# Optimization experiments

Measured on AMD Instinct MI355X. Metric: run time of the kernel, lower is better.

Reference implementation:

```python
import jax, jax.numpy as jnp
import numpy as np

B, CI, CO, K, SD, H, W = 8, 128, 128, 3, 512, 256, 256


def setup_inputs() -> dict:
    key = jax.random.key(0)
    k0, k1, k2, k3 = jax.random.split(key, 4)
    x = jax.random.normal(k0, (B, CI, H, W), jnp.float32)
    style = jax.random.normal(k1, (B, SD), jnp.float32)
    # learned params
    w_base = jax.random.normal(k2, (1, CO, CI, K, K), jnp.float32)   # ModulatedConv2d.weight
    aff_w = jax.random.normal(k3, (CI, SD), jnp.float32)             # affine weight [out=CI, in=SD]
    aff_b = jnp.ones((CI,), jnp.float32)                             # bias_init=1
    return {"x": x, "style": style, "w_base": w_base, "aff_w": aff_w, "aff_b": aff_b}


def reference(x, style, w_base, aff_w, aff_b):
    b, ci, h, w_ = x.shape
    co, k = w_base.shape[1], w_base.shape[3]
    # affine: FullyConnectedLayer, linear activation, weight_gain = 1/sqrt(style_dim)
    aff_gain = 1.0 / np.sqrt(aff_w.shape[1])
    s = style @ (aff_w * aff_gain).T + aff_b                 # [B, CI]
    # modulate
    wgain = 1.0 / np.sqrt(ci * k * k)
    wt = w_base * wgain * s[:, None, :, None, None]          # [B, CO, CI, K, K]
    # demodulate
    d = jax.lax.rsqrt(jnp.sum(wt * wt, axis=(2, 3, 4)) + 1e-8)  # [B, CO]
    wt = wt * d[:, :, None, None, None]
    # grouped conv, groups = batch, padding = k//2 (up=down=1 path)
    wt = wt.reshape(b * co, ci, k, k)
    xg = x.reshape(1, b * ci, h, w_)
    pad = k // 2
    y = jax.lax.conv_general_dilated(
        xg, wt, window_strides=(1, 1), padding=[(pad, pad), (pad, pad)],
        dimension_numbers=("NCHW", "OIHW", "NCHW"), feature_group_count=b)
    return y.reshape(b, co, h, w_)
```

## Files before the change

kernel.cpp:

```cpp
#include <hip/hip_runtime.h>
#include <stdint.h>

#define BB 8
#define SD 512
#define PP 66564

typedef unsigned short u16;
typedef __attribute__((ext_vector_type(8))) __bf16 bf16x8;
typedef __attribute__((ext_vector_type(16))) float f32x16;

__device__ float g_s[BB * 128];
__device__ u16 g_wtb[BB * 9 * 2 * 8192];
__device__ u16 g_xb[(size_t)BB * 258 * 258 * 128 + 2048];

typedef const __attribute__((address_space(1))) uint32_t* gp1;
typedef __attribute__((address_space(3))) uint32_t* lp3;

__device__ __forceinline__ void glds16(const void* g, void* l) {
    __builtin_amdgcn_global_load_lds((gp1)g, (lp3)l, 16, 0, 0);
}
__device__ __forceinline__ void glds4(const void* g, void* l) {
    __builtin_amdgcn_global_load_lds((gp1)g, (lp3)l, 4, 0, 0);
}

__device__ __forceinline__ u16 f2bf(float f) {
    uint32_t u = __float_as_uint(f);
    u += 0x7FFFu + ((u >> 16) & 1u);
    return (u16)(u >> 16);
}

__global__ void affine_kernel(const float* __restrict__ style,
                              const float* __restrict__ aff_w,
                              const float* __restrict__ aff_b) {
    int b = blockIdx.x;
    int ci = threadIdx.x;
    const float gain = 0.044194173824159216f;
    const float* st = style + b * SD;
    const float* aw = aff_w + ci * SD;
    float acc = 0.f;
    #pragma unroll 8
    for (int j = 0; j < SD; ++j) acc += st[j] * aw[j];
    g_s[b * 128 + ci] = acc * gain + aff_b[ci];
}

__global__ __launch_bounds__(256) void modulate_kernel(const float* __restrict__ w_base) {
    int blk = blockIdx.x;
    int b = blk >> 7, co = blk & 127;
    int tid = threadIdx.x;
    const float wgain = 0.029462782549439483f;
    const int n = 1152;
    const float* wb = w_base + co * n;
    const float* sp = g_s + b * 128;

    float v[5];
    float sq = 0.f;
    #pragma unroll
    for (int i = 0; i < 5; ++i) {
        int idx = tid + i * 256;
        float w = 0.f;
        if (idx < n) {
            int ci = idx / 9;
            w = wb[idx] * wgain * sp[ci];
        }
        v[i] = w;
        sq += w * w;
    }
    #pragma unroll
    for (int off = 32; off > 0; off >>= 1) sq += __shfl_down(sq, off, 64);
    __shared__ float red[4];
    int lane = tid & 63, wvi = tid >> 6;
    if (lane == 0) red[wvi] = sq;
    __syncthreads();
    float tot = red[0] + red[1] + red[2] + red[3];
    float d = rsqrtf(tot + 1e-8f);
    #pragma unroll
    for (int i = 0; i < 5; ++i) {
        int idx = tid + i * 256;
        if (idx < n) {
            int ci = idx / 9;
            int k9 = idx - ci * 9;
            u16 hv = f2bf(v[i] * d);
            int slot = (ci & 63) >> 3, e = ci & 7;
            size_t base = ((size_t)(b * 9 + k9) * 2 + (ci >> 6)) * 8192;
            g_wtb[base + slot * 1024 + co * 8 + e] = hv;
        }
    }
}

__global__ __launch_bounds__(256) void zero_border_kernel() {
    int b = blockIdx.x;
    uint4 z = make_uint4(0, 0, 0, 0);
    char* xbB = (char*)g_xb;
    for (int i = threadIdx.x; i < 16448; i += 256) {
        int plane = i / 1028, rem = i - plane * 1028;
        int gy, gx;
        if (rem < 258)      { gy = 0;             gx = rem; }
        else if (rem < 516) { gy = 257;           gx = rem - 258; }
        else if (rem < 772) { gy = rem - 516 + 1; gx = 0; }
        else                { gy = rem - 772 + 1; gx = 257; }
        size_t a16 = (size_t)(b * 16 + plane) * PP + (size_t)gy * 258 + gx;
        *(uint4*)(xbB + a16 * 16) = z;
    }
}

__global__ __launch_bounds__(256) void transpose_kernel(const float* __restrict__ x) {
    __shared__ __align__(16) u16 t_lds[64 * 128];
    const int chunk = blockIdx.x;
    const int gy = blockIdx.y;
    const int b = blockIdx.z;
    const int px0 = chunk * 64;
    const int tid = threadIdx.x;
    const int pq = tid & 15;
    const int cig = tid >> 4;

    const float* base = x + (size_t)b * 128 * 65536 + (size_t)gy * 256 + px0 + pq * 4;
    char* ldsB = (char*)t_lds;

    float4 v[8];
    #pragma unroll
    for (int c = 0; c < 8; ++c)
        v[c] = *(const float4*)(base + (size_t)(cig * 8 + c) * 65536);

    #pragma unroll
    for (int j = 0; j < 4; ++j) {
        uint32_t dw[4];
        #pragma unroll
        for (int d = 0; d < 4; ++d) {
            const float* lo4 = (const float*)&v[2 * d];
            const float* hi4 = (const float*)&v[2 * d + 1];
            dw[d] = (uint32_t)f2bf(lo4[j]) | ((uint32_t)f2bf(hi4[j]) << 16);
        }
        int px = pq * 4 + j;
        int key = (px0 + px + 1) & 7;
        int slot = cig ^ key;
        *(uint4*)(ldsB + px * 256 + slot * 16) = *(uint4*)dw;
    }
    __syncthreads();

    char* outB = (char*)g_xb;
    #pragma unroll
    for (int it = 0; it < 4; ++it) {
        int flat = it * 256 + tid;
        int r = flat >> 4, k = flat & 15;
        int key = (px0 + r + 1) & 7;
        uint4 val = *(const uint4*)(ldsB + r * 256 + ((k ^ key) << 4));
        size_t a16 = (size_t)(b * 16 + k) * PP + (size_t)(gy + 1) * 258 + (px0 + r + 1);
        *(uint4*)(outB + a16 * 16) = val;
    }
}

__global__ __launch_bounds__(512, 4) void conv_kernel(float* __restrict__ y) {
    __shared__ __align__(16) u16 xs[2720 * 8];
    __shared__ __align__(16) u16 ab[2][8192];

    const int b = blockIdx.y;
    const int t = blockIdx.x;
    const int swzt = (t & 7) * 32 + (t >> 3);
    const int tx = swzt & 7, ty = swzt >> 3;
    const int y0 = ty * 8, x0 = tx * 32;
    const int tid = threadIdx.x;
    const int lane = tid & 63, wv = tid >> 6;
    const int l31 = lane & 31;
    const int l5 = lane >> 5;
    const int coHalf = (wv & 1) * 64;
    const int py0w = (wv >> 1) * 2;

    const char* xbB = (const char*)g_xb;
    const char* wtbB = (const char*)(g_wtb) + (size_t)b * 294912;
    char* xsB = (char*)xs;

    f32x16 acc[2][2];
    #pragma unroll
    for (int mf = 0; mf < 2; ++mf)
        #pragma unroll
        for (int rf = 0; rf < 2; ++rf)
            acc[mf][rf] = (f32x16){0.f};

    for (int h = 0; h < 2; ++h) {
        for (int i = wv; i < 44; i += 8) {
            if (i < 42) {
                int entry = i * 64 + lane;
                int slot = entry / 340;
                int rem = entry - slot * 340;
                int row = rem / 34;
                int col = rem - row * 34;
                size_t a16 = (size_t)(b * 16 + h * 8 + slot) * PP +
                             (size_t)(y0 + row) * 258 + (x0 + col);
                glds16(xbB + a16 * 16, xsB + i * 1024);
            } else {
                int j = i - 42;
                int entry = 2688 + j * 16 + (lane >> 2);
                int rem = entry - 2380;
                int row = rem / 34;
                int col = rem - row * 34;
                size_t a16 = (size_t)(b * 16 + h * 8 + 7) * PP +
                             (size_t)(y0 + row) * 258 + (x0 + col);
                glds4(xbB + a16 * 16 + (lane & 3) * 4, xsB + 43008 + j * 256);
            }
        }
        if (h == 0) {
            #pragma unroll
            for (int q = 0; q < 2; ++q) {
                int j = wv * 2 + q;
                glds16(wtbB + j * 1024 + lane * 16, (char*)ab[0] + j * 1024);
            }
        }
        __syncthreads();

        for (int tap = 0; tap < 9; ++tap) {
            int s = h * 9 + tap;
            if (s < 17) {
                int ns = s + 1;
                int ntap = (ns >= 9) ? (ns - 9) : ns;
                int nh = (ns >= 9) ? 1 : h;
                const char* src = wtbB + (ntap * 2 + nh) * 16384;
                char* dst = (char*)ab[ns & 1];
                #pragma unroll
                for (int q = 0; q < 2; ++q) {
                    int j = wv * 2 + q;
                    glds16(src + j * 1024 + lane * 16, dst + j * 1024);
                }
            }

            const int ky = tap / 3, kx = tap - ky * 3;
            const char* abuf = (const char*)ab[s & 1];
            const int brow = (py0w + ky) * 34 + l31 + kx;

            #pragma unroll
            for (int ks = 0; ks < 4; ++ks) {
                const int cig = ks * 2 + l5;
                bf16x8 af[2];
                #pragma unroll
                for (int mf = 0; mf < 2; ++mf) {
                    int co = coHalf + mf * 32 + l31;
                    af[mf] = *(const bf16x8*)(abuf + cig * 2048 + co * 16);
                }
                bf16x8 bf[2];
                #pragma unroll
                for (int rf = 0; rf < 2; ++rf)
                    bf[rf] = *(const bf16x8*)(xsB + (cig * 340 + brow + rf * 34) * 16);
                __builtin_amdgcn_s_setprio(1);
                #pragma unroll
                for (int mf = 0; mf < 2; ++mf)
                    #pragma unroll
                    for (int rf = 0; rf < 2; ++rf)
                        acc[mf][rf] = __builtin_amdgcn_mfma_f32_32x32x16_bf16(
                            af[mf], bf[rf], acc[mf][rf], 0, 0, 0);
                __builtin_amdgcn_s_setprio(0);
            }
            __syncthreads();
        }
    }

    float* yb = y + (size_t)b * 128 * 65536;
    #pragma unroll
    for (int mf = 0; mf < 2; ++mf) {
        #pragma unroll
        for (int rf = 0; rf < 2; ++rf) {
            int gy = y0 + py0w + rf;
            int gx = x0 + l31;
            #pragma unroll
            for (int j = 0; j < 16; ++j) {
                int co = coHalf + mf * 32 + (j & 3) + 8 * (j >> 2) + 4 * l5;
                yb[(size_t)co * 65536 + gy * 256 + gx] = acc[mf][rf][j];
            }
        }
    }
}

extern "C" void kernel_launch(void* const* d_in, const int* in_sizes, int n_in,
                              void* d_out, int out_size, void* d_ws, size_t ws_size,
                              hipStream_t stream) {
    const float* x = (const float*)d_in[0];
    const float* style = (const float*)d_in[1];
    const float* w_base = (const float*)d_in[2];
    const float* aff_w = (const float*)d_in[3];
    const float* aff_b = (const float*)d_in[4];
    float* y = (float*)d_out;

    affine_kernel<<<BB, 128, 0, stream>>>(style, aff_w, aff_b);
    modulate_kernel<<<BB * 128, 256, 0, stream>>>(w_base);
    zero_border_kernel<<<BB, 256, 0, stream>>>();
    transpose_kernel<<<dim3(4, 256, BB), 256, 0, stream>>>(x);
    conv_kernel<<<dim3(256, BB), 512, 0, stream>>>(y);
}
```

Measured before the change: 389.5 us.

## Store padded bf16 input as pixel-major NHWC instead of channel-slot planes

Changes the intermediate bf16 input buffer from 16 separate per-slot planes of 16-byte channel groups to a pixel-major layout, with all 128 channels (256 bytes) of a pixel stored contiguously. The transpose writes, border zeroing and the conv kernel's global-to-LDS loads are updated to match. The goal is better locality: the transpose writes become contiguous per pixel, and conv tile loads touch fewer distinct DRAM pages. The trade-off is that each conv load wave now reads 16-byte chunks at a 256-byte stride within a row, so coalescing per instruction may be worse.

New measurement: 408.3 us. 4.8% more time.

```diff
diff --git a/kernel.cpp b/kernel.cpp
--- a/kernel.cpp
+++ b/kernel.cpp
@@ -3,7 +3,6 @@
 
 #define BB 8
 #define SD 512
-#define PP 66564
 
 typedef unsigned short u16;
 typedef __attribute__((ext_vector_type(8))) __bf16 bf16x8;
@@ -92,14 +91,12 @@
     uint4 z = make_uint4(0, 0, 0, 0);
     char* xbB = (char*)g_xb;
     for (int i = threadIdx.x; i < 16448; i += 256) {
-        int plane = i / 1028, rem = i - plane * 1028;
-        int gy, gx;
-        if (rem < 258)      { gy = 0;             gx = rem; }
-        else if (rem < 516) { gy = 257;           gx = rem - 258; }
-        else if (rem < 772) { gy = rem - 516 + 1; gx = 0; }
-        else                { gy = rem - 772 + 1; gx = 257; }
-        size_t a16 = (size_t)(b * 16 + plane) * PP + (size_t)gy * 258 + gx;
-        *(uint4*)(xbB + a16 * 16) = z;
+        size_t pix; int k;
+        if (i < 4128)       { pix = (size_t)(b * 258 + 0)   * 258 + (i >> 4);            k = i & 15; }
+        else if (i < 8256)  { int j = i - 4128;  pix = (size_t)(b * 258 + 257) * 258 + (j >> 4);       k = j & 15; }
+        else if (i < 12352) { int j = i - 8256;  pix = (size_t)(b * 258 + 1 + (j >> 4)) * 258 + 0;     k = j & 15; }
+        else                { int j = i - 12352; pix = (size_t)(b * 258 + 1 + (j >> 4)) * 258 + 257;   k = j & 15; }
+        *(uint4*)(xbB + pix * 256 + (size_t)k * 16) = z;
     }
 }
 
@@ -144,8 +141,8 @@
         int r = flat >> 4, k = flat & 15;
         int key = (px0 + r + 1) & 7;
         uint4 val = *(const uint4*)(ldsB + r * 256 + ((k ^ key) << 4));
-        size_t a16 = (size_t)(b * 16 + k) * PP + (size_t)(gy + 1) * 258 + (px0 + r + 1);
-        *(uint4*)(outB + a16 * 16) = val;
+        size_t pix = ((size_t)(b * 258 + gy + 1)) * 258 + (px0 + r + 1);
+        *(uint4*)(outB + pix * 256 + k * 16) = val;
     }
 }
 
@@ -184,18 +181,17 @@
                 int rem = entry - slot * 340;
                 int row = rem / 34;
                 int col = rem - row * 34;
-                size_t a16 = (size_t)(b * 16 + h * 8 + slot) * PP +
-                             (size_t)(y0 + row) * 258 + (x0 + col);
-                glds16(xbB + a16 * 16, xsB + i * 1024);
+                size_t pix = (size_t)(b * 258 + y0 + row) * 258 + (x0 + col);
+                glds16(xbB + pix * 256 + h * 128 + slot * 16, xsB + i * 1024);
             } else {
                 int j = i - 42;
                 int entry = 2688 + j * 16 + (lane >> 2);
                 int rem = entry - 2380;
                 int row = rem / 34;
                 int col = rem - row * 34;
-                size_t a16 = (size_t)(b * 16 + h * 8 + 7) * PP +
-                             (size_t)(y0 + row) * 258 + (x0 + col);
-                glds4(xbB + a16 * 16 + (lane & 3) * 4, xsB + 43008 + j * 256);
+                size_t pix = (size_t)(b * 258 + y0 + row) * 258 + (x0 + col);
+                glds4(xbB + pix * 256 + h * 128 + 112 + (lane & 3) * 4,
+                      xsB + 43008 + j * 256);
             }
         }
         if (h == 0) {
```
